# Performance work log

Hardware: AMD Instinct MI355X
Metric: run time of the kernel (lower is better)

The kernel has to match this reference:

```python
import jax, jax.numpy as jnp
import numpy as np

BRANCH = 8
LEVELS = 7
N = (BRANCH ** LEVELS - 1) // (BRANCH - 1)  # 299593 nodes, complete 8-ary tree
VOCAB, IN_DIM, MEM = 50000, 300, 150


def _tree_structure():
    parent = np.empty(N, np.int32)
    parent[0] = N  # sentinel: root scatters into dropped segment N
    idx = np.arange(1, N)
    parent[1:] = (idx - 1) // BRANCH
    depth = np.empty(N, np.int32)
    start = 0
    for d in range(LEVELS):
        cnt = BRANCH ** d
        depth[start:start + cnt] = d
        start += cnt
    return jnp.asarray(parent), jnp.asarray(depth)


def setup_inputs() -> dict:
    key = jax.random.key(0)
    ks = jax.random.split(key, 20)
    parent, depth = _tree_structure()
    inp = {
        'tokens': jax.random.randint(ks[0], (N,), 0, VOCAB, dtype=jnp.int32),
        'parent': parent,
        'depth': depth,
        'max_depth': LEVELS,
        'emb': jax.random.normal(ks[1], (VOCAB, IN_DIM), jnp.float32) * 0.1,
    }
    names_x = ['Wix', 'Wfx', 'Wox', 'Wux']
    names_h = ['Wih', 'Wfh', 'Woh', 'Wuh']
    sx = 1.0 / np.sqrt(IN_DIM)
    sh = 1.0 / np.sqrt(MEM)
    for j, (nx, nh) in enumerate(zip(names_x, names_h)):
        inp[nx] = jax.random.normal(ks[2 + 4 * j], (MEM, IN_DIM), jnp.float32) * sx
        inp['b' + nx[1:]] = jax.random.normal(ks[3 + 4 * j], (MEM,), jnp.float32) * sx
        inp[nh] = jax.random.normal(ks[4 + 4 * j], (MEM, MEM), jnp.float32) * sh
        inp['b' + nh[1:]] = jax.random.normal(ks[5 + 4 * j], (MEM,), jnp.float32) * sh
    return inp


def reference(tokens, parent, depth, max_depth, emb,
              Wix, bix, Wih, bih, Wfx, bfx, Wfh, bfh,
              Wox, box, Woh, boh, Wux, bux, Wuh, buh):
    n = tokens.shape[0]
    x = emb[tokens]  # [N, in_dim]
    # precompute all input-side gate projections once (batched GEMMs)
    ix_x = x @ Wix.T + bix
    fx_x = x @ Wfx.T + bfx
    ox_x = x @ Wox.T + box
    ux_x = x @ Wux.T + bux
    # parent index safe for gathering (root's sentinel -> 0; its row is masked out)
    gparent = jnp.where(parent >= n, 0, parent)

    h = jnp.zeros((n, MEM), x.dtype)
    c = jnp.zeros((n, MEM), x.dtype)

    # level-synchronous bottom-up sweep (loop over tree depth, not data)
    for d in range(max_depth - 1, -1, -1):
        # per-child forget gate: sigmoid(fh(h_child) + fx(x_parent)) * c_child
        f = jax.nn.sigmoid(h @ Wfh.T + bfh + fx_x[gparent])
        fc_sum = jax.ops.segment_sum(f * c, parent, num_segments=n + 1)[:n]
        h_sum = jax.ops.segment_sum(h, parent, num_segments=n + 1)[:n]
        i = jax.nn.sigmoid(ix_x + h_sum @ Wih.T + bih)
        o = jax.nn.sigmoid(ox_x + h_sum @ Woh.T + boh)
        u = jnp.tanh(ux_x + h_sum @ Wuh.T + buh)
        c_new = i * u + fc_sum
        h_new = o * jnp.tanh(c_new)
        mask = (depth == d)[:, None]
        c = jnp.where(mask, c_new, c)
        h = jnp.where(mask, h_new, h)
    # original returns concatenated cell states (post-order); here indexed by node id
    return c
```

## Files before the change

### kernel.cpp

```cpp
#include <hip/hip_runtime.h>


#define MEMD  150
#define IND   300
#define NINT  37449
#define VOCAB 50000
#define GROW  600
#define FSTR  152

typedef short bf16x8 __attribute__((ext_vector_type(8)));
typedef float f32x16 __attribute__((ext_vector_type(16)));
#define ZERO16 {0,0,0,0,0,0,0,0,0,0,0,0,0,0,0,0}

#define GALL_OFF 0ul
#define FHX_OFF  60000000ul
#define HSB_OFF  67600000ul
#define FCS_OFF  79000000ul
#define BPX_OFF  90400000ul
#define BPH_OFF  90800000ul

__device__ __forceinline__ float b2f(unsigned short u) {
    union { unsigned int i; float f; } v; v.i = ((unsigned int)u) << 16; return v.f;
}
__device__ __forceinline__ unsigned short f2b(float f) {
    union { float f; unsigned int i; } v; v.f = f;
    unsigned int x = v.i;
    x += 0x7fffu + ((x >> 16) & 1u);
    return (unsigned short)(x >> 16);
}
__device__ __forceinline__ float sigm(float x) {
    return __builtin_amdgcn_rcpf(1.0f + __expf(-x));
}
__device__ __forceinline__ float tanh_fast(float x) {
    float e = __expf(2.0f * x);
    return 1.0f - 2.0f * __builtin_amdgcn_rcpf(e + 1.0f);
}
__device__ __forceinline__ unsigned char f2e4m3(float f) {
    union { float f; unsigned u; } v; v.f = f;
    unsigned s = (v.u >> 31) << 7;
    float af = fabsf(f);
    if (af >= 448.f) return (unsigned char)(s | 0x7E);
    if (af < 0.015625f) {
        int m = (int)(af * 512.f + 0.5f);
        if (m > 7) m = 7;
        return (unsigned char)(s | m);
    }
    unsigned u = v.u & 0x7fffffffu;
    u += 0x7ffffu + ((u >> 20) & 1u);
    int ef = (int)(u >> 23) - 120;
    unsigned m = (u >> 20) & 7u;
    if (ef < 1) { ef = 1; m = 0; }
    if (ef > 15) { ef = 15; m = 6; }
    return (unsigned char)(s | (ef << 3) | m);
}
__device__ __forceinline__ float e4m3f(unsigned char u) {
    unsigned s = (u >> 7) & 1u, ef = (u >> 3) & 15u, m = u & 7u;
    if (ef == 0) {
        float r = (float)m * 0.001953125f;
        return s ? -r : r;
    }
    union { unsigned u; float f; } v;
    v.u = (s << 31) | ((ef + 120) << 23) | (m << 20);
    return v.f;
}

__global__ void pack_w(const float* __restrict__ Wix, const float* __restrict__ Wox,
                       const float* __restrict__ Wux, const float* __restrict__ Wfx,
                       const float* __restrict__ Wih, const float* __restrict__ Woh,
                       const float* __restrict__ Wuh, const float* __restrict__ Wfh,
                       unsigned short* __restrict__ bpx, unsigned short* __restrict__ bph)
{
    const int total_x = 4 * 5 * 19 * 512;
    const int total_h = 4 * 5 * 10 * 512;
    for (int i = blockIdx.x * blockDim.x + threadIdx.x; i < total_x + total_h;
         i += gridDim.x * blockDim.x) {
        if (i < total_x) {
            int e = i & 7, lane = (i >> 3) & 63, rest = i >> 9;
            int ks = rest % 19; rest /= 19;
            int nt = rest % 5;  int g = rest / 5;
            int col = nt * 32 + (lane & 31);
            int k = ks * 16 + ((lane >> 5) << 3) + e;
            const float* W = (g == 0) ? Wix : (g == 1) ? Wox : (g == 2) ? Wux : Wfx;
            bpx[i] = f2b((col < MEMD && k < IND) ? W[col * IND + k] : 0.f);
        } else {
            int j = i - total_x;
            int e = j & 7, lane = (j >> 3) & 63, rest = j >> 9;
            int ks = rest % 10; rest /= 10;
            int nt = rest % 5;  int g = rest / 5;
            int col = nt * 32 + (lane & 31);
            int k = ks * 16 + ((lane >> 5) << 3) + e;
            const float* W = (g == 0) ? Wih : (g == 1) ? Woh : (g == 2) ? Wuh : Wfh;
            bph[j] = f2b((col < MEMD && k < MEMD) ? W[col * MEMD + k] : 0.f);
        }
    }
}

__global__ __launch_bounds__(640, 2)
void vocab_gemm(const float* __restrict__ emb,
                const float* __restrict__ bix, const float* __restrict__ bih,
                const float* __restrict__ box_, const float* __restrict__ boh,
                const float* __restrict__ bux, const float* __restrict__ buh,
                const float* __restrict__ bfx, const float* __restrict__ bfh,
                const unsigned short* __restrict__ bpx_u,
                unsigned short* __restrict__ gall)
{
    __shared__ __align__(16) char sm0[40960];
    const int tid = threadIdx.x, lane = tid & 63, w = tid >> 6;
    const int hi = lane >> 5, ln31 = lane & 31;
    const int tile0 = blockIdx.x * 64;
    const int rowsValid = min(64, VOCAB - tile0);
    const int mt = (w >= 5) ? 1 : 0, nt = w - mt * 5;

    for (int i = tid; i < 64 * 40; i += 640) {
        int r = i / 40, q = i % 40;
        int rr = (r < rowsValid) ? r : 0;
        const float* er = emb + (long)(tile0 + rr) * IND;
        float4 v0 = {0.f,0.f,0.f,0.f}, v1 = {0.f,0.f,0.f,0.f};
        if (q < 38) v0 = *(const float4*)(er + q * 8);
        if (q < 37) v1 = *(const float4*)(er + q * 8 + 4);
        bf16x8 p;
        p[0]=(short)f2b(v0.x); p[1]=(short)f2b(v0.y); p[2]=(short)f2b(v0.z); p[3]=(short)f2b(v0.w);
        p[4]=(short)f2b(v1.x); p[5]=(short)f2b(v1.y); p[6]=(short)f2b(v1.z); p[7]=(short)f2b(v1.w);
        *(bf16x8*)(sm0 + r * 640 + ((q * 16) ^ ((r & 7) << 4))) = p;
    }
    __syncthreads();

    const bf16x8* BX = (const bf16x8*)bpx_u;
    const int row = mt * 32 + ln31;
    const int col = nt * 32 + ln31;
    const bool colv = col < MEMD;
    const int cc = colv ? col : 0;
    const float* b1[4] = {bix, box_, bux, bfx};
    const float* b2[4] = {bih, boh, buh, bfh};

    for (int g = 0; g < 4; ++g) {
        f32x16 acc = ZERO16;
        bf16x8 aC = *(const bf16x8*)(sm0 + row * 640 + ((hi * 16) ^ ((row & 7) << 4)));
        bf16x8 bC = BX[((g * 5 + nt) * 19 + 0) * 64 + lane];
        #pragma unroll
        for (int ks = 0; ks < 19; ++ks) {
            bf16x8 aN, bN;
            if (ks < 18) {
                aN = *(const bf16x8*)(sm0 + row * 640 + (((ks + 1) * 32 + hi * 16) ^ ((row & 7) << 4)));
                bN = BX[((g * 5 + nt) * 19 + ks + 1) * 64 + lane];
            }
            acc = __builtin_amdgcn_mfma_f32_32x32x16_bf16(aC, bC, acc, 0, 0, 0);
            aC = aN; bC = bN;
        }
        float bias = colv ? (b1[g][cc] + b2[g][cc]) : 0.f;
        #pragma unroll
        for (int r = 0; r < 16; ++r) {
            int rloc = mt * 32 + (r & 3) + 8 * (r >> 2) + 4 * hi;
            if (rloc < rowsValid && colv)
                gall[(long)(tile0 + rloc) * GROW + col * 4 + g] = f2b(acc[r] + bias);
        }
    }
}

__global__ __launch_bounds__(256, 8)
void hleaf_k(const unsigned short* __restrict__ gall, unsigned short* __restrict__ htmp)
{
    int i = blockIdx.x * 256 + threadIdx.x;
    if (i >= VOCAB * FSTR) return;
    int v = i / FSTR, col = i % FSTR;
    unsigned short r = 0;
    if (col < MEMD) {
        ushort4 gv = *(const ushort4*)(gall + (long)v * GROW + col * 4);
        float iv = sigm(b2f(gv.x));
        float ov = sigm(b2f(gv.y));
        float uv = tanh_fast(b2f(gv.z));
        float cv = iv * uv;
        r = f2b(ov * tanh_fast(cv));
    }
    htmp[i] = r;
}

__global__ __launch_bounds__(320, 4)
void fhx_gemm(const unsigned short* __restrict__ htmp,
              const unsigned short* __restrict__ bph_u,
              unsigned char* __restrict__ fhx)
{
    __shared__ __align__(16) char sm0[12288];
    const int tid = threadIdx.x, lane = tid & 63, w = tid >> 6;
    const int hi = lane >> 5, ln31 = lane & 31;
    const int tile0 = blockIdx.x * 32;
    const int rowsValid = min(32, VOCAB - tile0);
    const int nt = w;

    for (int i = tid; i < 32 * 20; i += 320) {
        int r = i / 20, q = i % 20;
        int rr = (r < rowsValid) ? r : 0;
        bf16x8 v = {0,0,0,0,0,0,0,0};
        if (q < 19) v = *(const bf16x8*)(htmp + (long)(tile0 + rr) * FSTR + q * 8);
        *(bf16x8*)(sm0 + r * 384 + ((q * 16) ^ ((r & 7) << 4))) = v;
    }
    __syncthreads();

    const bf16x8* BH = (const bf16x8*)bph_u;
    const int row = ln31;
    f32x16 ff = ZERO16;
    #pragma unroll
    for (int ks = 0; ks < 10; ++ks) {
        bf16x8 a = *(const bf16x8*)(sm0 + row * 384 + ((ks * 32 + hi * 16) ^ ((row & 7) << 4)));
        ff = __builtin_amdgcn_mfma_f32_32x32x16_bf16(a, BH[((15 + nt) * 10 + ks) * 64 + lane], ff, 0, 0, 0);
    }
    const int col = nt * 32 + ln31;
    if (col < MEMD) {
        #pragma unroll
        for (int r = 0; r < 16; ++r) {
            int rloc = (r & 3) + 8 * (r >> 2) + 4 * hi;
            if (rloc < rowsValid)
                fhx[(long)(tile0 + rloc) * FSTR + col] = f2e4m3(ff[r]);
        }
    }
}

__global__ __launch_bounds__(320, 8)
void leaf_csum(const int* __restrict__ tokens,
               const unsigned short* __restrict__ gall,
               const unsigned char* __restrict__ fhx,
               unsigned short* __restrict__ hsumb, unsigned short* __restrict__ fcs,
               float* __restrict__ c_out)
{
    __shared__ int ctok[16];
    __shared__ int ptokL[2];
    const int tid = threadIdx.x;
    const int pl = tid / 160;
    const int col0 = tid % 160;
    const bool colv = col0 < MEMD;
    const int col = colv ? col0 : (MEMD - 1);
    const int pidx = blockIdx.x * 2 + pl;
    const int pnode = 4681 + pidx;
    const long cbase = 8L * pnode + 1;
    if (tid < 16) ctok[tid] = tokens[37449 + blockIdx.x * 16 + tid];
    if (tid < 2)  ptokL[tid] = tokens[4681 + blockIdx.x * 2 + tid];
    __syncthreads();

    const float fxp = b2f(gall[(long)ptokL[pl] * GROW + col * 4 + 3]);
    float hs = 0.f, fc = 0.f;
    #pragma unroll
    for (int k = 0; k < 8; ++k) {
        int ct = ctok[pl * 8 + k];
        ushort4 gv = *(const ushort4*)(gall + (long)ct * GROW + col * 4);
        float iv = sigm(b2f(gv.x));
        float ov = sigm(b2f(gv.y));
        float uv = tanh_fast(b2f(gv.z));
        float cv = iv * uv;
        float h = ov * tanh_fast(cv);
        float f = sigm(e4m3f(fhx[(long)ct * FSTR + col]) + fxp);
        hs += h;
        fc += f * cv;
        if (colv) c_out[(cbase + k) * MEMD + col] = cv;
    }
    if (colv) {
        hsumb[(long)pnode * FSTR + col] = f2b(hs);
        fcs[(long)pnode * FSTR + col]  = f2b(fc);
    }
}

__global__ __launch_bounds__(320, 2)
void level_k(const int* __restrict__ tokens,
             const unsigned short* __restrict__ gall,
             const unsigned short* __restrict__ bph_u,
             unsigned short* __restrict__ hsumb, unsigned short* __restrict__ fcsum,
             float* __restrict__ c_out, int base, int cnt, int writePar)
{
    __shared__ __align__(16) char sm0[24576];
    __shared__ int toksL[32];
    __shared__ int ptokL[4];
    const int tid = threadIdx.x, lane = tid & 63, w = tid >> 6;
    const int hi = lane >> 5, ln31 = lane & 31;
    const int tile0 = blockIdx.x * 32;
    const int nodeBase = base + tile0;
    const int rowsValid = min(32, cnt - tile0);
    const int p0 = (nodeBase - 1) >> 3;
    const int nt = w;

    if (tid < 32) toksL[tid] = tokens[nodeBase + ((tid < rowsValid) ? tid : 0)];
    if (writePar && tid < 4) ptokL[tid] = tokens[p0 + tid];
    for (int i = tid; i < 32 * 20; i += 320) {
        int r = i / 20, q = i % 20;
        int rr = (r < rowsValid) ? r : 0;
        bf16x8 v = {0,0,0,0,0,0,0,0};
        if (q < 19)
            v = *(const bf16x8*)(hsumb + (long)(nodeBase + rr) * FSTR + q * 8);
        *(bf16x8*)(sm0 + 12288 + r * 384 + ((q * 16) ^ ((r & 7) << 4))) = v;
    }
    __syncthreads();

    const bf16x8* BH = (const bf16x8*)bph_u;
    const int row = ln31;
    const int col = nt * 32 + ln31;
    const bool colv = col < MEMD;
    const int cc = colv ? col : 0;

    f32x16 ai = ZERO16, ao = ZERO16, au = ZERO16;
    {
        const char* hb = sm0 + 12288;
        bf16x8 aC = *(const bf16x8*)(hb + row * 384 + ((hi * 16) ^ ((row & 7) << 4)));
        bf16x8 b0C = BH[((0 * 5 + nt) * 10 + 0) * 64 + lane];
        bf16x8 b1C = BH[((1 * 5 + nt) * 10 + 0) * 64 + lane];
        bf16x8 b2C = BH[((2 * 5 + nt) * 10 + 0) * 64 + lane];
        #pragma unroll
        for (int ks = 0; ks < 10; ++ks) {
            bf16x8 aN, b0N, b1N, b2N;
            if (ks < 9) {
                aN  = *(const bf16x8*)(hb + row * 384 + (((ks + 1) * 32 + hi * 16) ^ ((row & 7) << 4)));
                b0N = BH[((0 * 5 + nt) * 10 + ks + 1) * 64 + lane];
                b1N = BH[((1 * 5 + nt) * 10 + ks + 1) * 64 + lane];
                b2N = BH[((2 * 5 + nt) * 10 + ks + 1) * 64 + lane];
            }
            ai = __builtin_amdgcn_mfma_f32_32x32x16_bf16(aC, b0C, ai, 0, 0, 0);
            ao = __builtin_amdgcn_mfma_f32_32x32x16_bf16(aC, b1C, ao, 0, 0, 0);
            au = __builtin_amdgcn_mfma_f32_32x32x16_bf16(aC, b2C, au, 0, 0, 0);
            aC = aN; b0C = b0N; b1C = b1N; b2C = b2N;
        }
    }

    float cvv[16];
    {
        float hp[4] = {0.f, 0.f, 0.f, 0.f};
        #pragma unroll
        for (int r = 0; r < 16; ++r) {
            int rloc = (r & 3) + 8 * (r >> 2) + 4 * hi;
            bool rv = rloc < rowsValid;
            ushort4 gv = *(const ushort4*)(gall + (long)toksL[rloc] * GROW + cc * 4);
            float fcin = (rv && colv) ? b2f(fcsum[(long)(nodeBase + rloc) * FSTR + col]) : 0.f;
            float iv = sigm(ai[r] + b2f(gv.x));
            float ov = sigm(ao[r] + b2f(gv.y));
            float uv = tanh_fast(au[r] + b2f(gv.z));
            float cv = iv * uv + fcin;
            float h = (rv && colv) ? ov * tanh_fast(cv) : 0.f;
            cvv[r] = (rv && colv) ? cv : 0.f;
            if (rv && colv) c_out[(long)(nodeBase + rloc) * MEMD + col] = cv;
            *(unsigned short*)(sm0 + rloc * 384 + ((col * 2) ^ ((rloc & 7) << 4))) = f2b(h);
            hp[r >> 2] += h;
        }
        if (writePar) {
            #pragma unroll
            for (int o = 0; o < 4; ++o) {
                float s = hp[o] + __shfl_xor(hp[o], 32);
                if (lane < 32 && colv && o * 8 < rowsValid)
                    hsumb[(long)(p0 + o) * FSTR + col] = f2b(s);
            }
        }
    }
    __syncthreads();

    if (writePar) {
        f32x16 ff = ZERO16;
        {
            bf16x8 aC = *(const bf16x8*)(sm0 + row * 384 + ((hi * 16) ^ ((row & 7) << 4)));
            bf16x8 bC = BH[((15 + nt) * 10 + 0) * 64 + lane];
            #pragma unroll
            for (int ks = 0; ks < 10; ++ks) {
                bf16x8 aN, bN;
                if (ks < 9) {
                    aN = *(const bf16x8*)(sm0 + row * 384 + (((ks + 1) * 32 + hi * 16) ^ ((row & 7) << 4)));
                    bN = BH[((15 + nt) * 10 + ks + 1) * 64 + lane];
                }
                ff = __builtin_amdgcn_mfma_f32_32x32x16_bf16(aC, bC, ff, 0, 0, 0);
                aC = aN; bC = bN;
            }
        }
        #pragma unroll
        for (int o = 0; o < 4; ++o) {
            float fx = b2f(gall[(long)ptokL[o] * GROW + cc * 4 + 3]);
            float fp = 0.f;
            #pragma unroll
            for (int q = 0; q < 4; ++q) {
                int r = o * 4 + q;
                fp += sigm(ff[r] + fx) * cvv[r];
            }
            float s = fp + __shfl_xor(fp, 32);
            if (lane < 32 && colv && o * 8 < rowsValid)
                fcsum[(long)(p0 + o) * FSTR + col] = f2b(s);
        }
    }
}

__global__ __launch_bounds__(320, 2)
void tail_k(const int* __restrict__ tokens,
            const unsigned short* __restrict__ gall,
            const unsigned short* __restrict__ bph_u,
            unsigned short* __restrict__ hsumb, unsigned short* __restrict__ fcsum,
            float* __restrict__ c_out)
{
    __shared__ __align__(16) char sm0[24576];
    __shared__ int toksL[32];
    __shared__ int ptokL[4];
    const int tid = threadIdx.x, lane = tid & 63, w = tid >> 6;
    const int hi = lane >> 5, ln31 = lane & 31;
    const int nt = w;
    const bf16x8* BH = (const bf16x8*)bph_u;
    const int row = ln31;
    const int col = nt * 32 + ln31;
    const bool colv = col < MEMD;
    const int cc = colv ? col : 0;

    const int basesL[3] = {9, 1, 0};
    const int cntsL[3]  = {64, 8, 1};
    const int wpL[3]    = {1, 1, 0};

    for (int li = 0; li < 3; ++li) {
        for (int t0 = 0; t0 < cntsL[li]; t0 += 32) {
            const int nodeBase = basesL[li] + t0;
            const int rowsValid = min(32, cntsL[li] - t0);
            const int p0 = (nodeBase - 1) >> 3;
            const int writePar = wpL[li];

            if (tid < 32) toksL[tid] = tokens[nodeBase + ((tid < rowsValid) ? tid : 0)];
            if (writePar && tid < 4) ptokL[tid] = tokens[p0 + tid];
            for (int i = tid; i < 32 * 20; i += 320) {
                int r = i / 20, q = i % 20;
                int rr = (r < rowsValid) ? r : 0;
                bf16x8 v = {0,0,0,0,0,0,0,0};
                if (q < 19)
                    v = *(const bf16x8*)(hsumb + (long)(nodeBase + rr) * FSTR + q * 8);
                *(bf16x8*)(sm0 + 12288 + r * 384 + ((q * 16) ^ ((r & 7) << 4))) = v;
            }
            __syncthreads();

            f32x16 ai = ZERO16, ao = ZERO16, au = ZERO16;
            {
                const char* hb = sm0 + 12288;
                #pragma unroll
                for (int ks = 0; ks < 10; ++ks) {
                    bf16x8 a = *(const bf16x8*)(hb + row * 384 + ((ks * 32 + hi * 16) ^ ((row & 7) << 4)));
                    ai = __builtin_amdgcn_mfma_f32_32x32x16_bf16(a, BH[((0 * 5 + nt) * 10 + ks) * 64 + lane], ai, 0, 0, 0);
                    ao = __builtin_amdgcn_mfma_f32_32x32x16_bf16(a, BH[((1 * 5 + nt) * 10 + ks) * 64 + lane], ao, 0, 0, 0);
                    au = __builtin_amdgcn_mfma_f32_32x32x16_bf16(a, BH[((2 * 5 + nt) * 10 + ks) * 64 + lane], au, 0, 0, 0);
                }
            }

            float cvv[16];
            {
                float hp[4] = {0.f, 0.f, 0.f, 0.f};
                #pragma unroll
                for (int r = 0; r < 16; ++r) {
                    int rloc = (r & 3) + 8 * (r >> 2) + 4 * hi;
                    bool rv = rloc < rowsValid;
                    ushort4 gv = *(const ushort4*)(gall + (long)toksL[rloc] * GROW + cc * 4);
                    float fcin = (rv && colv) ? b2f(fcsum[(long)(nodeBase + rloc) * FSTR + col]) : 0.f;
                    float iv = sigm(ai[r] + b2f(gv.x));
                    float ov = sigm(ao[r] + b2f(gv.y));
                    float uv = tanh_fast(au[r] + b2f(gv.z));
                    float cv = iv * uv + fcin;
                    float h = (rv && colv) ? ov * tanh_fast(cv) : 0.f;
                    cvv[r] = (rv && colv) ? cv : 0.f;
                    if (rv && colv) c_out[(long)(nodeBase + rloc) * MEMD + col] = cv;
                    *(unsigned short*)(sm0 + rloc * 384 + ((col * 2) ^ ((rloc & 7) << 4))) = f2b(h);
                    hp[r >> 2] += h;
                }
                if (writePar) {
                    #pragma unroll
                    for (int o = 0; o < 4; ++o) {
                        float s = hp[o] + __shfl_xor(hp[o], 32);
                        if (lane < 32 && colv && o * 8 < rowsValid)
                            hsumb[(long)(p0 + o) * FSTR + col] = f2b(s);
                    }
                }
            }
            __syncthreads();

            if (writePar) {
                f32x16 ff = ZERO16;
                #pragma unroll
                for (int ks = 0; ks < 10; ++ks) {
                    bf16x8 a = *(const bf16x8*)(sm0 + row * 384 + ((ks * 32 + hi * 16) ^ ((row & 7) << 4)));
                    ff = __builtin_amdgcn_mfma_f32_32x32x16_bf16(a, BH[((15 + nt) * 10 + ks) * 64 + lane], ff, 0, 0, 0);
                }
                #pragma unroll
                for (int o = 0; o < 4; ++o) {
                    float fx = b2f(gall[(long)ptokL[o] * GROW + cc * 4 + 3]);
                    float fp = 0.f;
                    #pragma unroll
                    for (int q = 0; q < 4; ++q)
                        fp += sigm(ff[o * 4 + q] + fx) * cvv[o * 4 + q];
                    float s = fp + __shfl_xor(fp, 32);
                    if (lane < 32 && colv && o * 8 < rowsValid)
                        fcsum[(long)(p0 + o) * FSTR + col] = f2b(s);
                }
            }
            __syncthreads();
        }
    }
}

extern "C" void kernel_launch(void* const* d_in, const int* in_sizes, int n_in,
                              void* d_out, int out_size, void* d_ws, size_t ws_size,
                              hipStream_t stream) {
    const int*   tokens = (const int*)d_in[0];
    const float* emb = (const float*)d_in[4];
    const float* Wix = (const float*)d_in[5];  const float* bix = (const float*)d_in[6];
    const float* Wih = (const float*)d_in[7];  const float* bih = (const float*)d_in[8];
    const float* Wfx = (const float*)d_in[9];  const float* bfx = (const float*)d_in[10];
    const float* Wfh = (const float*)d_in[11]; const float* bfh = (const float*)d_in[12];
    const float* Wox = (const float*)d_in[13]; const float* box_ = (const float*)d_in[14];
    const float* Woh = (const float*)d_in[15]; const float* boh = (const float*)d_in[16];
    const float* Wux = (const float*)d_in[17]; const float* bux = (const float*)d_in[18];
    const float* Wuh = (const float*)d_in[19]; const float* buh = (const float*)d_in[20];
    float* c_out = (float*)d_out;
    char* ws = (char*)d_ws;

    unsigned short* gall  = (unsigned short*)(ws + GALL_OFF);
    unsigned char*  fhx   = (unsigned char*)(ws + FHX_OFF);
    unsigned short* hsumb = (unsigned short*)(ws + HSB_OFF);
    unsigned short* htmp  = (unsigned short*)(ws + HSB_OFF);
    unsigned short* fcs   = (unsigned short*)(ws + FCS_OFF);
    unsigned short* bpx   = (unsigned short*)(ws + BPX_OFF);
    unsigned short* bph   = (unsigned short*)(ws + BPH_OFF);

    pack_w<<<128, 512, 0, stream>>>(Wix, Wox, Wux, Wfx, Wih, Woh, Wuh, Wfh, bpx, bph);
    vocab_gemm<<<(VOCAB + 63) / 64, 640, 0, stream>>>(
        emb, bix, bih, box_, boh, bux, buh, bfx, bfh, bpx, gall);
    hleaf_k<<<(VOCAB * FSTR + 255) / 256, 256, 0, stream>>>(gall, htmp);
    fhx_gemm<<<(VOCAB + 31) / 32, 320, 0, stream>>>(htmp, bph, fhx);
    leaf_csum<<<16384, 320, 0, stream>>>(tokens, gall, fhx, hsumb, fcs, c_out);

    static const int bases[7] = {0, 1, 9, 73, 585, 4681, 37449};
    static const int cnts[7]  = {1, 8, 64, 512, 4096, 32768, 262144};
    for (int d = 5; d >= 3; --d) {
        int grid = (cnts[d] + 31) / 32;
        level_k<<<grid, 320, 0, stream>>>(
            tokens, gall, bph, hsumb, fcs, c_out, bases[d], cnts[d], 1);
    }
    tail_k<<<1, 320, 0, stream>>>(tokens, gall, bph, hsumb, fcs, c_out);
}
```

Measured before the change: 332.7 us.

## Fuse vocab GEMM, leaf activations and forget-hidden GEMM into one kernel

The vocab GEMM, the leaf h computation and the fh GEMM become one kernel. It computes all four gates per 32-row tile, derives the leaf c and h per vocabulary entry, stages h in shared memory and runs the Wfh MFMA in place. This removes two launches and the round trip of the h temp buffer. Leaf nodes now read the precomputed c and h instead of redoing the transcendentals for every child, and the leaf c_out writes move to a separate coalesced scatter kernel. The per-vocab intermediates live in parts of the output buffer that are overwritten later, which depends on the launch order being kept.

```diff
diff --git a/kernel.cpp b/kernel.cpp
--- a/kernel.cpp
+++ b/kernel.cpp
@@ -13,11 +13,14 @@
 #define ZERO16 {0,0,0,0,0,0,0,0,0,0,0,0,0,0,0,0}
 
 #define GALL_OFF 0ul
-#define FHX_OFF  60000000ul
-#define HSB_OFF  67600000ul
-#define FCS_OFF  79000000ul
-#define BPX_OFF  90400000ul
-#define BPH_OFF  90800000ul
+#define HSB_OFF  60000000ul
+#define FCS_OFF  71400000ul
+#define BPX_OFF  82800000ul
+#define BPH_OFF  83200000ul
+
+#define CLF_OUT_OFF 0ul
+#define HLF_OUT_OFF 22469504ul
+#define FHX_OUT_OFF 37669504ul
 
 __device__ __forceinline__ float b2f(unsigned short u) {
     union { unsigned int i; float f; } v; v.i = ((unsigned int)u) << 16; return v.f;
@@ -95,23 +98,26 @@
     }
 }
 
-__global__ __launch_bounds__(640, 2)
-void vocab_gemm(const float* __restrict__ emb,
-                const float* __restrict__ bix, const float* __restrict__ bih,
-                const float* __restrict__ box_, const float* __restrict__ boh,
-                const float* __restrict__ bux, const float* __restrict__ buh,
-                const float* __restrict__ bfx, const float* __restrict__ bfh,
-                const unsigned short* __restrict__ bpx_u,
-                unsigned short* __restrict__ gall)
+__global__ __launch_bounds__(320, 4)
+void vocab_all(const float* __restrict__ emb,
+               const float* __restrict__ bix, const float* __restrict__ bih,
+               const float* __restrict__ box_, const float* __restrict__ boh,
+               const float* __restrict__ bux, const float* __restrict__ buh,
+               const float* __restrict__ bfx, const float* __restrict__ bfh,
+               const unsigned short* __restrict__ bpx_u,
+               const unsigned short* __restrict__ bph_u,
+               unsigned short* __restrict__ gall,
+               unsigned short* __restrict__ cleaf,
+               unsigned short* __restrict__ hleaf,
+               unsigned char* __restrict__ fhx)
 {
-    __shared__ __align__(16) char sm0[40960];
+    __shared__ __align__(16) char sm0[32768];
     const int tid = threadIdx.x, lane = tid & 63, w = tid >> 6;
     const int hi = lane >> 5, ln31 = lane & 31;
-    const int tile0 = blockIdx.x * 64;
-    const int rowsValid = min(64, VOCAB - tile0);
-    const int mt = (w >= 5) ? 1 : 0, nt = w - mt * 5;
-
-    for (int i = tid; i < 64 * 40; i += 640) {
+    const int tile0 = blockIdx.x * 32;
+    const int rowsValid = min(32, VOCAB - tile0);
+
+    for (int i = tid; i < 32 * 40; i += 320) {
         int r = i / 40, q = i % 40;
         int rr = (r < rowsValid) ? r : 0;
         const float* er = emb + (long)(tile0 + rr) * IND;
@@ -126,86 +132,78 @@
     __syncthreads();
 
     const bf16x8* BX = (const bf16x8*)bpx_u;
-    const int row = mt * 32 + ln31;
+    const bf16x8* BH = (const bf16x8*)bph_u;
+    const int row = ln31, nt = w;
     const int col = nt * 32 + ln31;
     const bool colv = col < MEMD;
     const int cc = colv ? col : 0;
-    const float* b1[4] = {bix, box_, bux, bfx};
-    const float* b2[4] = {bih, boh, buh, bfh};
-
-    for (int g = 0; g < 4; ++g) {
-        f32x16 acc = ZERO16;
+
+    f32x16 a0 = ZERO16, a1 = ZERO16, a2 = ZERO16, a3 = ZERO16;
+    {
         bf16x8 aC = *(const bf16x8*)(sm0 + row * 640 + ((hi * 16) ^ ((row & 7) << 4)));
-        bf16x8 bC = BX[((g * 5 + nt) * 19 + 0) * 64 + lane];
+        bf16x8 b0C = BX[((0 * 5 + nt) * 19 + 0) * 64 + lane];
+        bf16x8 b1C = BX[((1 * 5 + nt) * 19 + 0) * 64 + lane];
+        bf16x8 b2C = BX[((2 * 5 + nt) * 19 + 0) * 64 + lane];
+        bf16x8 b3C = BX[((3 * 5 + nt) * 19 + 0) * 64 + lane];
         #pragma unroll
         for (int ks = 0; ks < 19; ++ks) {
+            bf16x8 aN, b0N, b1N, b2N, b3N;
+            if (ks < 18) {
+                aN  = *(const bf16x8*)(sm0 + row * 640 + (((ks + 1) * 32 + hi * 16) ^ ((row & 7) << 4)));
+                b0N = BX[((0 * 5 + nt) * 19 + ks + 1) * 64 + lane];
+                b1N = BX[((1 * 5 + nt) * 19 + ks + 1) * 64 + lane];
+                b2N = BX[((2 * 5 + nt) * 19 + ks + 1) * 64 + lane];
+                b3N = BX[((3 * 5 + nt) * 19 + ks + 1) * 64 + lane];
+            }
+            a0 = __builtin_amdgcn_mfma_f32_32x32x16_bf16(aC, b0C, a0, 0, 0, 0);
+            a1 = __builtin_amdgcn_mfma_f32_32x32x16_bf16(aC, b1C, a1, 0, 0, 0);
+            a2 = __builtin_amdgcn_mfma_f32_32x32x16_bf16(aC, b2C, a2, 0, 0, 0);
+            a3 = __builtin_amdgcn_mfma_f32_32x32x16_bf16(aC, b3C, a3, 0, 0, 0);
+            aC = aN; b0C = b0N; b1C = b1N; b2C = b2N; b3C = b3N;
+        }
+    }
+    const float bi = bix[cc] + bih[cc];
+    const float bo = box_[cc] + boh[cc];
+    const float bu = bux[cc] + buh[cc];
+    const float bf = bfx[cc] + bfh[cc];
+    #pragma unroll
+    for (int r = 0; r < 16; ++r) {
+        int rloc = (r & 3) + 8 * (r >> 2) + 4 * hi;
+        float pi = a0[r] + bi, po = a1[r] + bo, pu = a2[r] + bu, pf = a3[r] + bf;
+        float iv = sigm(pi);
+        float ov = sigm(po);
+        float uv = tanh_fast(pu);
+        float cv = iv * uv;
+        float hv = ov * tanh_fast(cv);
+        if (rloc < rowsValid && colv) {
+            long vrow = (long)(tile0 + rloc);
+            ushort4 g4;
+            g4.x = f2b(pi); g4.y = f2b(po); g4.z = f2b(pu); g4.w = f2b(pf);
+            *(ushort4*)(gall + vrow * GROW + col * 4) = g4;
+            cleaf[vrow * FSTR + col] = f2b(cv);
+            hleaf[vrow * FSTR + col] = f2b(hv);
+        }
+        *(unsigned short*)(sm0 + 20480 + rloc * 384 + ((col * 2) ^ ((rloc & 7) << 4))) = f2b(hv);
+    }
+    __syncthreads();
+
+    f32x16 ff = ZERO16;
+    {
+        const char* hb = sm0 + 20480;
+        bf16x8 aC = *(const bf16x8*)(hb + row * 384 + ((hi * 16) ^ ((row & 7) << 4)));
+        bf16x8 bC = BH[((15 + nt) * 10 + 0) * 64 + lane];
+        #pragma unroll
+        for (int ks = 0; ks < 10; ++ks) {
             bf16x8 aN, bN;
-            if (ks < 18) {
-                aN = *(const bf16x8*)(sm0 + row * 640 + (((ks + 1) * 32 + hi * 16) ^ ((row & 7) << 4)));
-                bN = BX[((g * 5 + nt) * 19 + ks + 1) * 64 + lane];
-            }
-            acc = __builtin_amdgcn_mfma_f32_32x32x16_bf16(aC, bC, acc, 0, 0, 0);
+            if (ks < 9) {
+                aN = *(const bf16x8*)(hb + row * 384 + (((ks + 1) * 32 + hi * 16) ^ ((row & 7) << 4)));
+                bN = BH[((15 + nt) * 10 + ks + 1) * 64 + lane];
+            }
+            ff = __builtin_amdgcn_mfma_f32_32x32x16_bf16(aC, bC, ff, 0, 0, 0);
             aC = aN; bC = bN;
         }
-        float bias = colv ? (b1[g][cc] + b2[g][cc]) : 0.f;
-        #pragma unroll
-        for (int r = 0; r < 16; ++r) {
-            int rloc = mt * 32 + (r & 3) + 8 * (r >> 2) + 4 * hi;
-            if (rloc < rowsValid && colv)
-                gall[(long)(tile0 + rloc) * GROW + col * 4 + g] = f2b(acc[r] + bias);
-        }
-    }
-}
-
-__global__ __launch_bounds__(256, 8)
-void hleaf_k(const unsigned short* __restrict__ gall, unsigned short* __restrict__ htmp)
-{
-    int i = blockIdx.x * 256 + threadIdx.x;
-    if (i >= VOCAB * FSTR) return;
-    int v = i / FSTR, col = i % FSTR;
-    unsigned short r = 0;
-    if (col < MEMD) {
-        ushort4 gv = *(const ushort4*)(gall + (long)v * GROW + col * 4);
-        float iv = sigm(b2f(gv.x));
-        float ov = sigm(b2f(gv.y));
-        float uv = tanh_fast(b2f(gv.z));
-        float cv = iv * uv;
-        r = f2b(ov * tanh_fast(cv));
-    }
-    htmp[i] = r;
-}
-
-__global__ __launch_bounds__(320, 4)
-void fhx_gemm(const unsigned short* __restrict__ htmp,
-              const unsigned short* __restrict__ bph_u,
-              unsigned char* __restrict__ fhx)
-{
-    __shared__ __align__(16) char sm0[12288];
-    const int tid = threadIdx.x, lane = tid & 63, w = tid >> 6;
-    const int hi = lane >> 5, ln31 = lane & 31;
-    const int tile0 = blockIdx.x * 32;
-    const int rowsValid = min(32, VOCAB - tile0);
-    const int nt = w;
-
-    for (int i = tid; i < 32 * 20; i += 320) {
-        int r = i / 20, q = i % 20;
-        int rr = (r < rowsValid) ? r : 0;
-        bf16x8 v = {0,0,0,0,0,0,0,0};
-        if (q < 19) v = *(const bf16x8*)(htmp + (long)(tile0 + rr) * FSTR + q * 8);
-        *(bf16x8*)(sm0 + r * 384 + ((q * 16) ^ ((r & 7) << 4))) = v;
-    }
-    __syncthreads();
-
-    const bf16x8* BH = (const bf16x8*)bph_u;
-    const int row = ln31;
-    f32x16 ff = ZERO16;
-    #pragma unroll
-    for (int ks = 0; ks < 10; ++ks) {
-        bf16x8 a = *(const bf16x8*)(sm0 + row * 384 + ((ks * 32 + hi * 16) ^ ((row & 7) << 4)));
-        ff = __builtin_amdgcn_mfma_f32_32x32x16_bf16(a, BH[((15 + nt) * 10 + ks) * 64 + lane], ff, 0, 0, 0);
-    }
-    const int col = nt * 32 + ln31;
-    if (col < MEMD) {
+    }
+    if (colv) {
         #pragma unroll
         for (int r = 0; r < 16; ++r) {
             int rloc = (r & 3) + 8 * (r >> 2) + 4 * hi;
@@ -216,11 +214,12 @@
 }
 
 __global__ __launch_bounds__(320, 8)
-void leaf_csum(const int* __restrict__ tokens,
-               const unsigned short* __restrict__ gall,
-               const unsigned char* __restrict__ fhx,
-               unsigned short* __restrict__ hsumb, unsigned short* __restrict__ fcs,
-               float* __restrict__ c_out)
+void leaf_sum(const int* __restrict__ tokens,
+              const unsigned short* __restrict__ gall,
+              const unsigned short* __restrict__ cleaf,
+              const unsigned short* __restrict__ hleaf,
+              const unsigned char* __restrict__ fhx,
+              unsigned short* __restrict__ hsumb, unsigned short* __restrict__ fcs)
 {
     __shared__ int ctok[16];
     __shared__ int ptokL[2];
@@ -229,9 +228,7 @@
     const int col0 = tid % 160;
     const bool colv = col0 < MEMD;
     const int col = colv ? col0 : (MEMD - 1);
-    const int pidx = blockIdx.x * 2 + pl;
-    const int pnode = 4681 + pidx;
-    const long cbase = 8L * pnode + 1;
+    const int pnode = 4681 + blockIdx.x * 2 + pl;
     if (tid < 16) ctok[tid] = tokens[37449 + blockIdx.x * 16 + tid];
     if (tid < 2)  ptokL[tid] = tokens[4681 + blockIdx.x * 2 + tid];
     __syncthreads();
@@ -241,21 +238,34 @@
     #pragma unroll
     for (int k = 0; k < 8; ++k) {
         int ct = ctok[pl * 8 + k];
-        ushort4 gv = *(const ushort4*)(gall + (long)ct * GROW + col * 4);
-        float iv = sigm(b2f(gv.x));
-        float ov = sigm(b2f(gv.y));
-        float uv = tanh_fast(b2f(gv.z));
-        float cv = iv * uv;
-        float h = ov * tanh_fast(cv);
-        float f = sigm(e4m3f(fhx[(long)ct * FSTR + col]) + fxp);
+        long o = (long)ct * FSTR + col;
+        float cv = b2f(cleaf[o]);
+        float h  = b2f(hleaf[o]);
+        float f  = sigm(e4m3f(fhx[o]) + fxp);
         hs += h;
         fc += f * cv;
-        if (colv) c_out[(cbase + k) * MEMD + col] = cv;
     }
     if (colv) {
         hsumb[(long)pnode * FSTR + col] = f2b(hs);
         fcs[(long)pnode * FSTR + col]  = f2b(fc);
     }
+}
+
+__global__ __launch_bounds__(256, 8)
+void leaf_scatter(const int* __restrict__ tokens,
+                  const unsigned short* __restrict__ cleaf,
+                  float* __restrict__ c_out)
+{
+    const long total = 262144L * 75;
+    long i = (long)blockIdx.x * 256 + threadIdx.x;
+    if (i >= total) return;
+    int n = (int)(i / 75), j = (int)(i % 75);
+    int tok = tokens[37449 + n];
+    unsigned int u = *(const unsigned int*)(cleaf + (long)tok * FSTR + j * 2);
+    float2 v;
+    v.x = b2f((unsigned short)(u & 0xffffu));
+    v.y = b2f((unsigned short)(u >> 16));
+    *(float2*)(c_out + (long)(37449 + n) * MEMD + j * 2) = v;
 }
 
 __global__ __launch_bounds__(320, 2)
@@ -404,19 +414,19 @@
 
     for (int li = 0; li < 3; ++li) {
         for (int t0 = 0; t0 < cntsL[li]; t0 += 32) {
-            const int nodeBase = basesL[li] + t0;
-            const int rowsValid = min(32, cntsL[li] - t0);
-            const int p0 = (nodeBase - 1) >> 3;
+            const int nb = basesL[li] + t0;
+            const int rv32 = min(32, cntsL[li] - t0);
+            const int pp0 = (nb - 1) >> 3;
             const int writePar = wpL[li];
 
-            if (tid < 32) toksL[tid] = tokens[nodeBase + ((tid < rowsValid) ? tid : 0)];
-            if (writePar && tid < 4) ptokL[tid] = tokens[p0 + tid];
+            if (tid < 32) toksL[tid] = tokens[nb + ((tid < rv32) ? tid : 0)];
+            if (writePar && tid < 4) ptokL[tid] = tokens[pp0 + tid];
             for (int i = tid; i < 32 * 20; i += 320) {
                 int r = i / 20, q = i % 20;
-                int rr = (r < rowsValid) ? r : 0;
+                int rr = (r < rv32) ? r : 0;
                 bf16x8 v = {0,0,0,0,0,0,0,0};
                 if (q < 19)
-                    v = *(const bf16x8*)(hsumb + (long)(nodeBase + rr) * FSTR + q * 8);
+                    v = *(const bf16x8*)(hsumb + (long)(nb + rr) * FSTR + q * 8);
                 *(bf16x8*)(sm0 + 12288 + r * 384 + ((q * 16) ^ ((r & 7) << 4))) = v;
             }
             __syncthreads();
@@ -439,16 +449,16 @@
                 #pragma unroll
                 for (int r = 0; r < 16; ++r) {
                     int rloc = (r & 3) + 8 * (r >> 2) + 4 * hi;
-                    bool rv = rloc < rowsValid;
+                    bool rv = rloc < rv32;
                     ushort4 gv = *(const ushort4*)(gall + (long)toksL[rloc] * GROW + cc * 4);
-                    float fcin = (rv && colv) ? b2f(fcsum[(long)(nodeBase + rloc) * FSTR + col]) : 0.f;
+                    float fcin = (rv && colv) ? b2f(fcsum[(long)(nb + rloc) * FSTR + col]) : 0.f;
                     float iv = sigm(ai[r] + b2f(gv.x));
                     float ov = sigm(ao[r] + b2f(gv.y));
                     float uv = tanh_fast(au[r] + b2f(gv.z));
                     float cv = iv * uv + fcin;
                     float h = (rv && colv) ? ov * tanh_fast(cv) : 0.f;
                     cvv[r] = (rv && colv) ? cv : 0.f;
-                    if (rv && colv) c_out[(long)(nodeBase + rloc) * MEMD + col] = cv;
+                    if (rv && colv) c_out[(long)(nb + rloc) * MEMD + col] = cv;
                     *(unsigned short*)(sm0 + rloc * 384 + ((col * 2) ^ ((rloc & 7) << 4))) = f2b(h);
                     hp[r >> 2] += h;
                 }
@@ -456,8 +466,8 @@
                     #pragma unroll
                     for (int o = 0; o < 4; ++o) {
                         float s = hp[o] + __shfl_xor(hp[o], 32);
-                        if (lane < 32 && colv && o * 8 < rowsValid)
-                            hsumb[(long)(p0 + o) * FSTR + col] = f2b(s);
+                        if (lane < 32 && colv && o * 8 < rv32)
+                            hsumb[(long)(pp0 + o) * FSTR + col] = f2b(s);
                     }
                 }
             }
@@ -478,8 +488,8 @@
                     for (int q = 0; q < 4; ++q)
                         fp += sigm(ff[o * 4 + q] + fx) * cvv[o * 4 + q];
                     float s = fp + __shfl_xor(fp, 32);
-                    if (lane < 32 && colv && o * 8 < rowsValid)
-                        fcsum[(long)(p0 + o) * FSTR + col] = f2b(s);
+                    if (lane < 32 && colv && o * 8 < rv32)
+                        fcsum[(long)(pp0 + o) * FSTR + col] = f2b(s);
                 }
             }
             __syncthreads();
@@ -502,25 +512,27 @@
     const float* Wuh = (const float*)d_in[19]; const float* buh = (const float*)d_in[20];
     float* c_out = (float*)d_out;
     char* ws = (char*)d_ws;
+    char* outb = (char*)d_out;
 
     unsigned short* gall  = (unsigned short*)(ws + GALL_OFF);
-    unsigned char*  fhx   = (unsigned char*)(ws + FHX_OFF);
     unsigned short* hsumb = (unsigned short*)(ws + HSB_OFF);
-    unsigned short* htmp  = (unsigned short*)(ws + HSB_OFF);
     unsigned short* fcs   = (unsigned short*)(ws + FCS_OFF);
     unsigned short* bpx   = (unsigned short*)(ws + BPX_OFF);
     unsigned short* bph   = (unsigned short*)(ws + BPH_OFF);
+    unsigned short* cleaf = (unsigned short*)(outb + CLF_OUT_OFF);
+    unsigned short* hleaf = (unsigned short*)(outb + HLF_OUT_OFF);
+    unsigned char*  fhx   = (unsigned char*)(outb + FHX_OUT_OFF);
 
     pack_w<<<128, 512, 0, stream>>>(Wix, Wox, Wux, Wfx, Wih, Woh, Wuh, Wfh, bpx, bph);
-    vocab_gemm<<<(VOCAB + 63) / 64, 640, 0, stream>>>(
-        emb, bix, bih, box_, boh, bux, buh, bfx, bfh, bpx, gall);
-    hleaf_k<<<(VOCAB * FSTR + 255) / 256, 256, 0, stream>>>(gall, htmp);
-    fhx_gemm<<<(VOCAB + 31) / 32, 320, 0, stream>>>(htmp, bph, fhx);
-    leaf_csum<<<16384, 320, 0, stream>>>(tokens, gall, fhx, hsumb, fcs, c_out);
-
-    static const int bases[7] = {0, 1, 9, 73, 585, 4681, 37449};
-    static const int cnts[7]  = {1, 8, 64, 512, 4096, 32768, 262144};
-    for (int d = 5; d >= 3; --d) {
+    vocab_all<<<(VOCAB + 31) / 32, 320, 0, stream>>>(
+        emb, bix, bih, box_, boh, bux, buh, bfx, bfh, bpx, bph,
+        gall, cleaf, hleaf, fhx);
+    leaf_sum<<<16384, 320, 0, stream>>>(tokens, gall, cleaf, hleaf, fhx, hsumb, fcs);
+    leaf_scatter<<<(int)((262144L * 75 + 255) / 256), 256, 0, stream>>>(tokens, cleaf, c_out);
+
+    static const int bases[3] = {4681, 585, 73};
+    static const int cnts[3]  = {32768, 4096, 512};
+    for (int d = 0; d < 3; ++d) {
         int grid = (cnts[d] + 31) / 32;
         level_k<<<grid, 320, 0, stream>>>(
             tokens, gall, bph, hsumb, fcs, c_out, bases[d], cnts[d], 1);
```

Measured after the change: 304.6 us. 1.09x faster.
